# Optimization experiments

Hardware: AMD Instinct MI355X
Metric: run time of the kernel (lower is better)

Reference implementation:

```python
import jax, jax.numpy as jnp
import numpy as np

P = 4        # number of sequence pairs (half batch)
L = 512      # sequence length
D = 64       # embedding dim
NUM_CLASSES = 4
BIAS_INIT = 10.0


def setup_inputs() -> dict:
    key = jax.random.key(0)
    k1, k2, k3 = jax.random.split(key, 3)
    seqs_logits = jax.random.normal(k1, (2 * P, L, D), dtype=jnp.float32)
    ordinal_weight = jax.random.normal(k2, (1, NUM_CLASSES), dtype=jnp.float32)
    ordinal_bias = jax.random.normal(k3, (NUM_CLASSES,), dtype=jnp.float32) + BIAS_INIT
    return {"seqs_logits": seqs_logits, "ordinal_weight": ordinal_weight,
            "ordinal_bias": ordinal_bias}


def reference(seqs_logits, ordinal_weight, ordinal_bias):
    half = seqs_logits.shape[0] // 2
    z0 = seqs_logits[:half]          # [P, L0, D]
    z1 = seqs_logits[half:2 * half]  # [P, L1, D]

    def score_plus(z0_i, z1_i):
        # pairwise negative L1 distance: [L0, L1]
        s = -jnp.sum(jnp.abs(z0_i[:, None, :] - z1_i[None, :, :]), axis=-1)
        a = jax.nn.softmax(s, axis=1)   # row-wise alignment
        b = jax.nn.softmax(s, axis=0)   # column-wise alignment
        c = a + b - a * b               # symmetric soft alignment
        c_val = jnp.sum(c * s) / jnp.sum(c)
        logit = c_val * ordinal_weight + ordinal_bias  # [1, 4]
        return logit.reshape(-1)        # [4]

    return jax.vmap(score_plus)(z0, z1)  # [P, 4]
```

## Files before the change

kernel.cpp:

```cpp
#include <hip/hip_runtime.h>
#include <math.h>

#define P 4
#define L 512
#define D 64
#define NC 4
#define RS 68
#define SHIFT 64.0f

#define COLP_O 0
#define ROWP_O 16384
#define BP_O   32768
#define SV_O   33280

__global__ __launch_bounds__(256) void dist_stats(const float* __restrict__ z,
                                                  float* __restrict__ ws) {
    const int bx = blockIdx.x;
    const int pair = bx >> 6, kb = (bx >> 3) & 7, jb = bx & 7;
    const int tid = threadIdx.x, tx = tid & 15, ty = tid >> 4;
    const int wave = tid >> 6, lane = tid & 63;

    __shared__ float jt[64][RS], kt[64][RS];
    __shared__ float csred[4][64];

    {
        const float4* z0t = (const float4*)(z + ((size_t)pair * L + jb * 64) * D);
        const float4* z1t = (const float4*)(z + ((size_t)(P + pair) * L + kb * 64) * D);
        #pragma unroll
        for (int i = 0; i < 4; ++i) {
            const int li = i * 256 + tid;
            const float4 a = z0t[li];
            const float4 b = z1t[li];
            *(float4*)&jt[li >> 4][(li & 15) * 4] = a;
            *(float4*)&kt[li >> 4][(li & 15) * 4] = b;
        }
    }
    __syncthreads();

    float acc[4][4];
    #pragma unroll
    for (int r = 0; r < 4; ++r)
        #pragma unroll
        for (int q = 0; q < 4; ++q) acc[r][q] = 0.f;
    #pragma unroll
    for (int c = 0; c < 16; ++c) {
        float4 jv[4], kv[4];
        #pragma unroll
        for (int r = 0; r < 4; ++r) jv[r] = *(const float4*)&jt[ty + 16 * r][c * 4];
        #pragma unroll
        for (int q = 0; q < 4; ++q) kv[q] = *(const float4*)&kt[tx + 16 * q][c * 4];
        #pragma unroll
        for (int r = 0; r < 4; ++r)
            #pragma unroll
            for (int q = 0; q < 4; ++q)
                acc[r][q] += fabsf(jv[r].x - kv[q].x) + fabsf(jv[r].y - kv[q].y)
                           + fabsf(jv[r].z - kv[q].z) + fabsf(jv[r].w - kv[q].w);
    }

    {
        float* svb = ws + SV_O + (size_t)bx * 4096;
        #pragma unroll
        for (int r = 0; r < 4; ++r)
            #pragma unroll
            for (int q = 0; q < 4; ++q)
                svb[(r * 4 + q) * 256 + tid] = -acc[r][q];
    }

    float rs_[4] = {0.f, 0.f, 0.f, 0.f};
    float cs_[4] = {0.f, 0.f, 0.f, 0.f};
    #pragma unroll
    for (int r = 0; r < 4; ++r)
        #pragma unroll
        for (int q = 0; q < 4; ++q) {
            const float e = __expf(SHIFT - acc[r][q]);
            rs_[r] += e;
            cs_[q] += e;
        }
    #pragma unroll
    for (int off = 1; off <= 8; off <<= 1)
        #pragma unroll
        for (int r = 0; r < 4; ++r) rs_[r] += __shfl_xor(rs_[r], off);
    if (tx == 0) {
        #pragma unroll
        for (int r = 0; r < 4; ++r)
            ws[ROWP_O + (pair * 8 + kb) * 512 + jb * 64 + ty + 16 * r] = rs_[r];
    }
    #pragma unroll
    for (int off = 16; off <= 32; off <<= 1)
        #pragma unroll
        for (int q = 0; q < 4; ++q) cs_[q] += __shfl_xor(cs_[q], off);
    if ((lane >> 4) == 0) {
        #pragma unroll
        for (int q = 0; q < 4; ++q) csred[wave][q * 16 + tx] = cs_[q];
    }
    __syncthreads();
    if (tid < 64)
        ws[COLP_O + (pair * 8 + jb) * 512 + kb * 64 + (tid & 15) + 16 * (tid >> 4)]
            = csred[0][tid] + csred[1][tid] + csred[2][tid] + csred[3][tid];
}

__global__ __launch_bounds__(256) void c_accum(const float* __restrict__ wsc,
                                               float* __restrict__ ws) {
    const int bx = blockIdx.x;
    const int pair = bx >> 6, kb = (bx >> 3) & 7, jb = bx & 7;
    const int tid = threadIdx.x, tx = tid & 15, ty = tid >> 4;
    const int wave = tid >> 6, lane = tid & 63;

    __shared__ float rtmp[64][4], ctmp[64][4];
    __shared__ float rrcp_s[64], crcp_s[64];
    __shared__ float bred[4][2];

    {
        const int l = tid >> 2, p4 = tid & 3;
        rtmp[l][p4] = wsc[ROWP_O + (pair * 8 + 2 * p4) * 512 + jb * 64 + l]
                    + wsc[ROWP_O + (pair * 8 + 2 * p4 + 1) * 512 + jb * 64 + l];
        ctmp[l][p4] = wsc[COLP_O + (pair * 8 + 2 * p4) * 512 + kb * 64 + l]
                    + wsc[COLP_O + (pair * 8 + 2 * p4 + 1) * 512 + kb * 64 + l];
    }
    __syncthreads();
    if (tid < 64) {
        rrcp_s[tid] = 1.0f / (rtmp[tid][0] + rtmp[tid][1] + rtmp[tid][2] + rtmp[tid][3]);
    } else if (tid < 128) {
        const int l = tid - 64;
        crcp_s[l] = 1.0f / (ctmp[l][0] + ctmp[l][1] + ctmp[l][2] + ctmp[l][3]);
    }
    __syncthreads();

    const float* svb = wsc + SV_O + (size_t)bx * 4096;
    float cs = 0.f, cc = 0.f;
    #pragma unroll
    for (int r = 0; r < 4; ++r) {
        const float rr = rrcp_s[ty + 16 * r];
        #pragma unroll
        for (int q = 0; q < 4; ++q) {
            const float cr = crcp_s[tx + 16 * q];
            const float sv = svb[(r * 4 + q) * 256 + tid];
            const float e  = __expf(SHIFT + sv);
            const float a  = e * rr;
            const float b  = e * cr;
            const float c  = a + b - a * b;
            cs += c * sv;
            cc += c;
        }
    }
    #pragma unroll
    for (int off = 1; off <= 32; off <<= 1) {
        cs += __shfl_xor(cs, off);
        cc += __shfl_xor(cc, off);
    }
    if (lane == 0) { bred[wave][0] = cs; bred[wave][1] = cc; }
    __syncthreads();
    if (tid == 0) {
        const int bidp = kb * 8 + jb;
        ws[BP_O + (pair * 64 + bidp) * 2]     = bred[0][0] + bred[1][0] + bred[2][0] + bred[3][0];
        ws[BP_O + (pair * 64 + bidp) * 2 + 1] = bred[0][1] + bred[1][1] + bred[2][1] + bred[3][1];
    }
}

__global__ __launch_bounds__(256) void finalize(const float* __restrict__ ws,
                                                const float* __restrict__ w,
                                                const float* __restrict__ bias,
                                                float* __restrict__ out) {
    const int tid = threadIdx.x;
    const int pair = tid >> 6, lane = tid & 63;
    float cs = ws[BP_O + (pair * 64 + lane) * 2];
    float cc = ws[BP_O + (pair * 64 + lane) * 2 + 1];
    #pragma unroll
    for (int off = 1; off <= 32; off <<= 1) {
        cs += __shfl_xor(cs, off);
        cc += __shfl_xor(cc, off);
    }
    if (lane == 0) {
        const float c_val = cs / cc;
        #pragma unroll
        for (int cls = 0; cls < NC; ++cls)
            out[pair * NC + cls] = c_val * w[cls] + bias[cls];
    }
}

extern "C" void kernel_launch(void* const* d_in, const int* in_sizes, int n_in,
                              void* d_out, int out_size, void* d_ws, size_t ws_size,
                              hipStream_t stream) {
    const float* z    = (const float*)d_in[0];
    const float* w    = (const float*)d_in[1];
    const float* bias = (const float*)d_in[2];
    float* out = (float*)d_out;
    float* ws  = (float*)d_ws;

    dist_stats<<<dim3(P * 64), dim3(256), 0, stream>>>(z, ws);
    c_accum   <<<dim3(P * 64), dim3(256), 0, stream>>>(ws, ws);
    finalize  <<<dim3(1),      dim3(256), 0, stream>>>(ws, w, bias, out);
}
```

Measured before the change: 68.72 us.

## Fuse three kernels into one persistent kernel with grid barriers

Merges dist_stats, c_accum and finalize into one kernel that uses two atomic-counter grid barriers. The score matrix stays in registers instead of being written to and re-read from the workspace. This removes two kernel launch gaps and several MB of global memory traffic. The barrier only works if all 256 blocks are resident at once. Its counter reset depends on the workspace holding a 0xAAAAAAAA fill pattern, which is fragile across repeated calls.

```diff
diff --git a/kernel.cpp b/kernel.cpp
--- a/kernel.cpp
+++ b/kernel.cpp
@@ -7,21 +7,49 @@
 #define NC 4
 #define RS 68
 #define SHIFT 64.0f
+#define NBLK (P * 64)
 
-#define COLP_O 0
-#define ROWP_O 16384
+#define ROWP_O 0
+#define COLP_O 16384
 #define BP_O   32768
-#define SV_O   33280
+#define CNT_O  33280
 
-__global__ __launch_bounds__(256) void dist_stats(const float* __restrict__ z,
-                                                  float* __restrict__ ws) {
+__device__ __forceinline__ void st_dev(float* p, float v) {
+    __hip_atomic_store(p, v, __ATOMIC_RELAXED, __HIP_MEMORY_SCOPE_AGENT);
+}
+__device__ __forceinline__ float ld_dev(const float* p) {
+    return __hip_atomic_load(p, __ATOMIC_RELAXED, __HIP_MEMORY_SCOPE_AGENT);
+}
+
+__device__ __forceinline__ void grid_barrier(int* cnt, int target, int tid) {
+    __syncthreads();
+    if (tid == 0) {
+        unsigned expected = 0xAAAAAAAAu;
+        __hip_atomic_compare_exchange_strong((unsigned*)cnt, &expected, 0u,
+            __ATOMIC_RELAXED, __ATOMIC_RELAXED, __HIP_MEMORY_SCOPE_AGENT);
+        __hip_atomic_fetch_add(cnt, 1, __ATOMIC_RELEASE, __HIP_MEMORY_SCOPE_AGENT);
+        while (__hip_atomic_load(cnt, __ATOMIC_ACQUIRE, __HIP_MEMORY_SCOPE_AGENT) < target)
+            __builtin_amdgcn_s_sleep(1);
+    }
+    __syncthreads();
+}
+
+__global__ __launch_bounds__(256) void ssa_one(const float* __restrict__ z,
+                                               const float* __restrict__ w,
+                                               const float* __restrict__ bias,
+                                               float* __restrict__ out,
+                                               float* __restrict__ ws) {
     const int bx = blockIdx.x;
     const int pair = bx >> 6, kb = (bx >> 3) & 7, jb = bx & 7;
     const int tid = threadIdx.x, tx = tid & 15, ty = tid >> 4;
     const int wave = tid >> 6, lane = tid & 63;
+    int* cnt = (int*)(ws + CNT_O);
 
     __shared__ float jt[64][RS], kt[64][RS];
     __shared__ float csred[4][64];
+    __shared__ float rtmp[64][4], ctmp[64][4];
+    __shared__ float rrcp_s[64], crcp_s[64];
+    __shared__ float bred[4][2];
 
     {
         const float4* z0t = (const float4*)(z + ((size_t)pair * L + jb * 64) * D);
@@ -57,15 +85,6 @@
                            + fabsf(jv[r].z - kv[q].z) + fabsf(jv[r].w - kv[q].w);
     }
 
-    {
-        float* svb = ws + SV_O + (size_t)bx * 4096;
-        #pragma unroll
-        for (int r = 0; r < 4; ++r)
-            #pragma unroll
-            for (int q = 0; q < 4; ++q)
-                svb[(r * 4 + q) * 256 + tid] = -acc[r][q];
-    }
-
     float rs_[4] = {0.f, 0.f, 0.f, 0.f};
     float cs_[4] = {0.f, 0.f, 0.f, 0.f};
     #pragma unroll
@@ -83,7 +102,7 @@
     if (tx == 0) {
         #pragma unroll
         for (int r = 0; r < 4; ++r)
-            ws[ROWP_O + (pair * 8 + kb) * 512 + jb * 64 + ty + 16 * r] = rs_[r];
+            st_dev(&ws[ROWP_O + (pair * 8 + kb) * 512 + jb * 64 + ty + 16 * r], rs_[r]);
     }
     #pragma unroll
     for (int off = 16; off <= 32; off <<= 1)
@@ -95,27 +114,17 @@
     }
     __syncthreads();
     if (tid < 64)
-        ws[COLP_O + (pair * 8 + jb) * 512 + kb * 64 + (tid & 15) + 16 * (tid >> 4)]
-            = csred[0][tid] + csred[1][tid] + csred[2][tid] + csred[3][tid];
-}
+        st_dev(&ws[COLP_O + (pair * 8 + jb) * 512 + kb * 64 + (tid & 15) + 16 * (tid >> 4)],
+               csred[0][tid] + csred[1][tid] + csred[2][tid] + csred[3][tid]);
 
-__global__ __launch_bounds__(256) void c_accum(const float* __restrict__ wsc,
-                                               float* __restrict__ ws) {
-    const int bx = blockIdx.x;
-    const int pair = bx >> 6, kb = (bx >> 3) & 7, jb = bx & 7;
-    const int tid = threadIdx.x, tx = tid & 15, ty = tid >> 4;
-    const int wave = tid >> 6, lane = tid & 63;
-
-    __shared__ float rtmp[64][4], ctmp[64][4];
-    __shared__ float rrcp_s[64], crcp_s[64];
-    __shared__ float bred[4][2];
+    grid_barrier(cnt, NBLK, tid);
 
     {
         const int l = tid >> 2, p4 = tid & 3;
-        rtmp[l][p4] = wsc[ROWP_O + (pair * 8 + 2 * p4) * 512 + jb * 64 + l]
-                    + wsc[ROWP_O + (pair * 8 + 2 * p4 + 1) * 512 + jb * 64 + l];
-        ctmp[l][p4] = wsc[COLP_O + (pair * 8 + 2 * p4) * 512 + kb * 64 + l]
-                    + wsc[COLP_O + (pair * 8 + 2 * p4 + 1) * 512 + kb * 64 + l];
+        rtmp[l][p4] = ld_dev(&ws[ROWP_O + (pair * 8 + 2 * p4) * 512 + jb * 64 + l])
+                    + ld_dev(&ws[ROWP_O + (pair * 8 + 2 * p4 + 1) * 512 + jb * 64 + l]);
+        ctmp[l][p4] = ld_dev(&ws[COLP_O + (pair * 8 + 2 * p4) * 512 + kb * 64 + l])
+                    + ld_dev(&ws[COLP_O + (pair * 8 + 2 * p4 + 1) * 512 + kb * 64 + l]);
     }
     __syncthreads();
     if (tid < 64) {
@@ -126,7 +135,6 @@
     }
     __syncthreads();
 
-    const float* svb = wsc + SV_O + (size_t)bx * 4096;
     float cs = 0.f, cc = 0.f;
     #pragma unroll
     for (int r = 0; r < 4; ++r) {
@@ -134,7 +142,7 @@
         #pragma unroll
         for (int q = 0; q < 4; ++q) {
             const float cr = crcp_s[tx + 16 * q];
-            const float sv = svb[(r * 4 + q) * 256 + tid];
+            const float sv = -acc[r][q];
             const float e  = __expf(SHIFT + sv);
             const float a  = e * rr;
             const float b  = e * cr;
@@ -151,30 +159,26 @@
     if (lane == 0) { bred[wave][0] = cs; bred[wave][1] = cc; }
     __syncthreads();
     if (tid == 0) {
-        const int bidp = kb * 8 + jb;
-        ws[BP_O + (pair * 64 + bidp) * 2]     = bred[0][0] + bred[1][0] + bred[2][0] + bred[3][0];
-        ws[BP_O + (pair * 64 + bidp) * 2 + 1] = bred[0][1] + bred[1][1] + bred[2][1] + bred[3][1];
+        st_dev(&ws[BP_O + bx * 2],     bred[0][0] + bred[1][0] + bred[2][0] + bred[3][0]);
+        st_dev(&ws[BP_O + bx * 2 + 1], bred[0][1] + bred[1][1] + bred[2][1] + bred[3][1]);
     }
-}
 
-__global__ __launch_bounds__(256) void finalize(const float* __restrict__ ws,
-                                                const float* __restrict__ w,
-                                                const float* __restrict__ bias,
-                                                float* __restrict__ out) {
-    const int tid = threadIdx.x;
-    const int pair = tid >> 6, lane = tid & 63;
-    float cs = ws[BP_O + (pair * 64 + lane) * 2];
-    float cc = ws[BP_O + (pair * 64 + lane) * 2 + 1];
-    #pragma unroll
-    for (int off = 1; off <= 32; off <<= 1) {
-        cs += __shfl_xor(cs, off);
-        cc += __shfl_xor(cc, off);
-    }
-    if (lane == 0) {
-        const float c_val = cs / cc;
+    grid_barrier(cnt + 1, NBLK, tid);
+
+    if (bx < P && tid < 64) {
+        float pcs = ld_dev(&ws[BP_O + (bx * 64 + tid) * 2]);
+        float pcc = ld_dev(&ws[BP_O + (bx * 64 + tid) * 2 + 1]);
         #pragma unroll
-        for (int cls = 0; cls < NC; ++cls)
-            out[pair * NC + cls] = c_val * w[cls] + bias[cls];
+        for (int off = 1; off <= 32; off <<= 1) {
+            pcs += __shfl_xor(pcs, off);
+            pcc += __shfl_xor(pcc, off);
+        }
+        if (tid == 0) {
+            const float c_val = pcs / pcc;
+            #pragma unroll
+            for (int cls = 0; cls < NC; ++cls)
+                out[bx * NC + cls] = c_val * w[cls] + bias[cls];
+        }
     }
 }
 
@@ -187,7 +191,5 @@
     float* out = (float*)d_out;
     float* ws  = (float*)d_ws;
 
-    dist_stats<<<dim3(P * 64), dim3(256), 0, stream>>>(z, ws);
-    c_accum   <<<dim3(P * 64), dim3(256), 0, stream>>>(ws, ws);
-    finalize  <<<dim3(1),      dim3(256), 0, stream>>>(ws, w, bias, out);
+    ssa_one<<<dim3(NBLK), dim3(256), 0, stream>>>(z, w, bias, out, ws);
 }
```

Result: slower. 88.26 us (+28.4%).

## Split distance tiles to 64x32 doubling block count and vectorize score stores

Applied to the files above, without the earlier changes.

Halves the column tile per block (64x32 instead of 64x64), giving 512 blocks instead of 256 so more CUs get work on the wide GPU. Each thread now holds a 2x4 accumulator and writes scores as contiguous float4. The row, column and block partial layouts, c_accum and finalize are reworked to match. The cost is more partial sums to reduce, a second load of the z0 tile per column half, and less register reuse per thread.

```diff
diff --git a/kernel.cpp b/kernel.cpp
--- a/kernel.cpp
+++ b/kernel.cpp
@@ -7,50 +7,56 @@
 #define NC 4
 #define RS 68
 #define SHIFT 64.0f
-
-#define COLP_O 0
-#define ROWP_O 16384
-#define BP_O   32768
-#define SV_O   33280
-
-__global__ __launch_bounds__(256) void dist_stats(const float* __restrict__ z,
-                                                  float* __restrict__ ws) {
+#define NBLK 512
+
+#define ROWP_O 0
+#define COLP_O 32768
+#define BP_O   49152
+#define SV_O   50176
+
+__global__ __launch_bounds__(256, 2) void dist_stats(const float* __restrict__ z,
+                                                     float* __restrict__ ws) {
     const int bx = blockIdx.x;
-    const int pair = bx >> 6, kb = (bx >> 3) & 7, jb = bx & 7;
-    const int tid = threadIdx.x, tx = tid & 15, ty = tid >> 4;
+    const int pair = bx >> 7, jb = (bx >> 4) & 7, kh = bx & 15;
+    const int tid = threadIdx.x;
+    const int tx = tid & 7;
+    const int ty = tid >> 3;
     const int wave = tid >> 6, lane = tid & 63;
 
-    __shared__ float jt[64][RS], kt[64][RS];
-    __shared__ float csred[4][64];
+    __shared__ float jt[64][RS];
+    __shared__ float kt[32][RS];
+    __shared__ float csred[4][32];
 
     {
         const float4* z0t = (const float4*)(z + ((size_t)pair * L + jb * 64) * D);
-        const float4* z1t = (const float4*)(z + ((size_t)(P + pair) * L + kb * 64) * D);
+        const float4* z1t = (const float4*)(z + ((size_t)(P + pair) * L + kh * 32) * D);
         #pragma unroll
         for (int i = 0; i < 4; ++i) {
             const int li = i * 256 + tid;
-            const float4 a = z0t[li];
-            const float4 b = z1t[li];
-            *(float4*)&jt[li >> 4][(li & 15) * 4] = a;
-            *(float4*)&kt[li >> 4][(li & 15) * 4] = b;
-        }
-    }
-    __syncthreads();
-
-    float acc[4][4];
-    #pragma unroll
-    for (int r = 0; r < 4; ++r)
+            *(float4*)&jt[li >> 4][(li & 15) * 4] = z0t[li];
+        }
+        #pragma unroll
+        for (int i = 0; i < 2; ++i) {
+            const int li = i * 256 + tid;
+            *(float4*)&kt[li >> 4][(li & 15) * 4] = z1t[li];
+        }
+    }
+    __syncthreads();
+
+    float acc[2][4];
+    #pragma unroll
+    for (int r = 0; r < 2; ++r)
         #pragma unroll
         for (int q = 0; q < 4; ++q) acc[r][q] = 0.f;
     #pragma unroll
     for (int c = 0; c < 16; ++c) {
-        float4 jv[4], kv[4];
-        #pragma unroll
-        for (int r = 0; r < 4; ++r) jv[r] = *(const float4*)&jt[ty + 16 * r][c * 4];
-        #pragma unroll
-        for (int q = 0; q < 4; ++q) kv[q] = *(const float4*)&kt[tx + 16 * q][c * 4];
-        #pragma unroll
-        for (int r = 0; r < 4; ++r)
+        float4 jv[2], kv[4];
+        #pragma unroll
+        for (int r = 0; r < 2; ++r) jv[r] = *(const float4*)&jt[ty + 32 * r][c * 4];
+        #pragma unroll
+        for (int q = 0; q < 4; ++q) kv[q] = *(const float4*)&kt[tx + 8 * q][c * 4];
+        #pragma unroll
+        for (int r = 0; r < 2; ++r)
             #pragma unroll
             for (int q = 0; q < 4; ++q)
                 acc[r][q] += fabsf(jv[r].x - kv[q].x) + fabsf(jv[r].y - kv[q].y)
@@ -58,18 +64,19 @@
     }
 
     {
-        float* svb = ws + SV_O + (size_t)bx * 4096;
-        #pragma unroll
-        for (int r = 0; r < 4; ++r)
-            #pragma unroll
-            for (int q = 0; q < 4; ++q)
-                svb[(r * 4 + q) * 256 + tid] = -acc[r][q];
-    }
-
-    float rs_[4] = {0.f, 0.f, 0.f, 0.f};
+        float4* svb = (float4*)(ws + SV_O + (size_t)bx * 2048 + tid * 8);
+        #pragma unroll
+        for (int r = 0; r < 2; ++r) {
+            float4 v;
+            v.x = -acc[r][0]; v.y = -acc[r][1]; v.z = -acc[r][2]; v.w = -acc[r][3];
+            svb[r] = v;
+        }
+    }
+
+    float rs_[2] = {0.f, 0.f};
     float cs_[4] = {0.f, 0.f, 0.f, 0.f};
     #pragma unroll
-    for (int r = 0; r < 4; ++r)
+    for (int r = 0; r < 2; ++r)
         #pragma unroll
         for (int q = 0; q < 4; ++q) {
             const float e = __expf(SHIFT - acc[r][q]);
@@ -77,64 +84,66 @@
             cs_[q] += e;
         }
     #pragma unroll
-    for (int off = 1; off <= 8; off <<= 1)
-        #pragma unroll
-        for (int r = 0; r < 4; ++r) rs_[r] += __shfl_xor(rs_[r], off);
+    for (int off = 1; off <= 4; off <<= 1)
+        #pragma unroll
+        for (int r = 0; r < 2; ++r) rs_[r] += __shfl_xor(rs_[r], off);
     if (tx == 0) {
         #pragma unroll
-        for (int r = 0; r < 4; ++r)
-            ws[ROWP_O + (pair * 8 + kb) * 512 + jb * 64 + ty + 16 * r] = rs_[r];
-    }
-    #pragma unroll
-    for (int off = 16; off <= 32; off <<= 1)
+        for (int r = 0; r < 2; ++r)
+            ws[ROWP_O + (pair * 16 + kh) * 512 + jb * 64 + ty + 32 * r] = rs_[r];
+    }
+    #pragma unroll
+    for (int off = 8; off <= 32; off <<= 1)
         #pragma unroll
         for (int q = 0; q < 4; ++q) cs_[q] += __shfl_xor(cs_[q], off);
-    if ((lane >> 4) == 0) {
-        #pragma unroll
-        for (int q = 0; q < 4; ++q) csred[wave][q * 16 + tx] = cs_[q];
-    }
-    __syncthreads();
-    if (tid < 64)
-        ws[COLP_O + (pair * 8 + jb) * 512 + kb * 64 + (tid & 15) + 16 * (tid >> 4)]
+    if (lane < 8) {
+        #pragma unroll
+        for (int q = 0; q < 4; ++q) csred[wave][tx + 8 * q] = cs_[q];
+    }
+    __syncthreads();
+    if (tid < 32)
+        ws[COLP_O + (pair * 8 + jb) * 512 + kh * 32 + tid]
             = csred[0][tid] + csred[1][tid] + csred[2][tid] + csred[3][tid];
 }
 
 __global__ __launch_bounds__(256) void c_accum(const float* __restrict__ wsc,
                                                float* __restrict__ ws) {
     const int bx = blockIdx.x;
-    const int pair = bx >> 6, kb = (bx >> 3) & 7, jb = bx & 7;
-    const int tid = threadIdx.x, tx = tid & 15, ty = tid >> 4;
+    const int pair = bx >> 7, jb = (bx >> 4) & 7, kh = bx & 15;
+    const int tid = threadIdx.x;
+    const int tx = tid & 7, ty = tid >> 3;
     const int wave = tid >> 6, lane = tid & 63;
 
-    __shared__ float rtmp[64][4], ctmp[64][4];
-    __shared__ float rrcp_s[64], crcp_s[64];
+    __shared__ float rrcp_s[64], crcp_s[32];
     __shared__ float bred[4][2];
 
-    {
-        const int l = tid >> 2, p4 = tid & 3;
-        rtmp[l][p4] = wsc[ROWP_O + (pair * 8 + 2 * p4) * 512 + jb * 64 + l]
-                    + wsc[ROWP_O + (pair * 8 + 2 * p4 + 1) * 512 + jb * 64 + l];
-        ctmp[l][p4] = wsc[COLP_O + (pair * 8 + 2 * p4) * 512 + kb * 64 + l]
-                    + wsc[COLP_O + (pair * 8 + 2 * p4 + 1) * 512 + kb * 64 + l];
-    }
-    __syncthreads();
     if (tid < 64) {
-        rrcp_s[tid] = 1.0f / (rtmp[tid][0] + rtmp[tid][1] + rtmp[tid][2] + rtmp[tid][3]);
-    } else if (tid < 128) {
-        const int l = tid - 64;
-        crcp_s[l] = 1.0f / (ctmp[l][0] + ctmp[l][1] + ctmp[l][2] + ctmp[l][3]);
-    }
-    __syncthreads();
-
-    const float* svb = wsc + SV_O + (size_t)bx * 4096;
+        float s = 0.f;
+        #pragma unroll
+        for (int h = 0; h < 16; ++h)
+            s += wsc[ROWP_O + (pair * 16 + h) * 512 + jb * 64 + tid];
+        rrcp_s[tid] = 1.0f / s;
+    } else if (tid < 96) {
+        const int kl = tid - 64;
+        float s = 0.f;
+        #pragma unroll
+        for (int b = 0; b < 8; ++b)
+            s += wsc[COLP_O + (pair * 8 + b) * 512 + kh * 32 + kl];
+        crcp_s[kl] = 1.0f / s;
+    }
+    __syncthreads();
+
+    const float4* svb = (const float4*)(wsc + SV_O + (size_t)bx * 2048 + tid * 8);
     float cs = 0.f, cc = 0.f;
     #pragma unroll
-    for (int r = 0; r < 4; ++r) {
-        const float rr = rrcp_s[ty + 16 * r];
+    for (int r = 0; r < 2; ++r) {
+        const float rr = rrcp_s[ty + 32 * r];
+        const float4 sv4 = svb[r];
+        const float svs[4] = {sv4.x, sv4.y, sv4.z, sv4.w};
         #pragma unroll
         for (int q = 0; q < 4; ++q) {
-            const float cr = crcp_s[tx + 16 * q];
-            const float sv = svb[(r * 4 + q) * 256 + tid];
+            const float cr = crcp_s[tx + 8 * q];
+            const float sv = svs[q];
             const float e  = __expf(SHIFT + sv);
             const float a  = e * rr;
             const float b  = e * cr;
@@ -151,30 +160,34 @@
     if (lane == 0) { bred[wave][0] = cs; bred[wave][1] = cc; }
     __syncthreads();
     if (tid == 0) {
-        const int bidp = kb * 8 + jb;
-        ws[BP_O + (pair * 64 + bidp) * 2]     = bred[0][0] + bred[1][0] + bred[2][0] + bred[3][0];
-        ws[BP_O + (pair * 64 + bidp) * 2 + 1] = bred[0][1] + bred[1][1] + bred[2][1] + bred[3][1];
-    }
-}
-
-__global__ __launch_bounds__(256) void finalize(const float* __restrict__ ws,
+        ws[BP_O + bx * 2]     = bred[0][0] + bred[1][0] + bred[2][0] + bred[3][0];
+        ws[BP_O + bx * 2 + 1] = bred[0][1] + bred[1][1] + bred[2][1] + bred[3][1];
+    }
+}
+
+__global__ __launch_bounds__(512) void finalize(const float* __restrict__ ws,
                                                 const float* __restrict__ w,
                                                 const float* __restrict__ bias,
                                                 float* __restrict__ out) {
     const int tid = threadIdx.x;
-    const int pair = tid >> 6, lane = tid & 63;
-    float cs = ws[BP_O + (pair * 64 + lane) * 2];
-    float cc = ws[BP_O + (pair * 64 + lane) * 2 + 1];
+    const int wave = tid >> 6, lane = tid & 63;
+    float cs = ws[BP_O + tid * 2];
+    float cc = ws[BP_O + tid * 2 + 1];
     #pragma unroll
     for (int off = 1; off <= 32; off <<= 1) {
         cs += __shfl_xor(cs, off);
         cc += __shfl_xor(cc, off);
     }
-    if (lane == 0) {
-        const float c_val = cs / cc;
+    __shared__ float red[8][2];
+    if (lane == 0) { red[wave][0] = cs; red[wave][1] = cc; }
+    __syncthreads();
+    if (tid < P) {
+        const float tcs = red[2 * tid][0] + red[2 * tid + 1][0];
+        const float tcc = red[2 * tid][1] + red[2 * tid + 1][1];
+        const float c_val = tcs / tcc;
         #pragma unroll
         for (int cls = 0; cls < NC; ++cls)
-            out[pair * NC + cls] = c_val * w[cls] + bias[cls];
+            out[tid * NC + cls] = c_val * w[cls] + bias[cls];
     }
 }
 
@@ -187,7 +200,7 @@
     float* out = (float*)d_out;
     float* ws  = (float*)d_ws;
 
-    dist_stats<<<dim3(P * 64), dim3(256), 0, stream>>>(z, ws);
-    c_accum   <<<dim3(P * 64), dim3(256), 0, stream>>>(ws, ws);
-    finalize  <<<dim3(1),      dim3(256), 0, stream>>>(ws, w, bias, out);
-}
+    dist_stats<<<dim3(NBLK), dim3(256), 0, stream>>>(z, ws);
+    c_accum   <<<dim3(NBLK), dim3(256), 0, stream>>>(ws, ws);
+    finalize  <<<dim3(1),    dim3(512), 0, stream>>>(ws, w, bias, out);
+}
```

Measured after the change: 69.64 us. About the same (+1.3%).
